# Kernel optimization log

Measured on AMD Instinct MI355X. Metric: run time of the kernel, lower is better.

The kernel has to match this reference:

```python
import jax, jax.numpy as jnp
import numpy as np

B, S, E, H = 4, 2048, 1024, 16
D = E // H  # head dim = 64


def setup_inputs() -> dict:
    key = jax.random.key(0)
    ks = jax.random.split(key, 9)
    s_in = 1.0 / np.sqrt(E)
    return {
        "x": jax.random.normal(ks[0], (B, S, E), dtype=jnp.float32),
        # stacked per-head projection weights, acting as x @ W + b
        "Wq": jax.random.normal(ks[1], (H, E, D), dtype=jnp.float32) * s_in,
        "bq": jax.random.normal(ks[2], (H, D), dtype=jnp.float32) * 0.01,
        "Wk": jax.random.normal(ks[3], (H, E, D), dtype=jnp.float32) * s_in,
        "bk": jax.random.normal(ks[4], (H, D), dtype=jnp.float32) * 0.01,
        "Wv": jax.random.normal(ks[5], (H, E, D), dtype=jnp.float32) * s_in,
        "bv": jax.random.normal(ks[6], (H, D), dtype=jnp.float32) * 0.01,
        "Wo": jax.random.normal(ks[7], (E, E), dtype=jnp.float32) * s_in,
        "bo": jax.random.normal(ks[8], (E,), dtype=jnp.float32) * 0.01,
    }


def reference(x, Wq, bq, Wk, bk, Wv, bv, Wo, bo):
    # Batched per-head projections (equivalent to the per-head nn.Linear loop)
    q = jnp.einsum("bse,hed->bhsd", x, Wq) + bq[None, :, None, :]
    k = jnp.einsum("bse,hed->bhsd", x, Wk) + bk[None, :, None, :]
    v = jnp.einsum("bse,hed->bhsd", x, Wv) + bv[None, :, None, :]
    scale = 1.0 / jnp.sqrt(jnp.asarray(D, dtype=x.dtype))
    scores = jnp.einsum("bhsd,bhtd->bhst", q, k) * scale  # [B,H,S,S]
    attn = jax.nn.softmax(scores, axis=-1)
    ctx = jnp.einsum("bhst,bhtd->bhsd", attn, v)  # [B,H,S,D]
    # torch.cat over heads along last dim -> [B,S,H*D]=[B,S,E]
    ctx = jnp.transpose(ctx, (0, 2, 1, 3)).reshape(x.shape[0], x.shape[1], E)
    return ctx @ Wo + bo
```

## Files before the change

### kernel.cpp

```cpp
#include <hip/hip_runtime.h>
#include <math.h>

#define B_ 4
#define S_ 2048
#define E_ 1024
#define H_ 16
#define D_ 64
#define BH_ (B_ * H_)

#define SCALE_LOG2E 0.18033688011112042f

typedef short short8 __attribute__((ext_vector_type(8)));
typedef float f32x4 __attribute__((ext_vector_type(4)));
typedef float f32x16 __attribute__((ext_vector_type(16)));

static __device__ __forceinline__ unsigned short f2bf(float f) {
    unsigned int u = __float_as_uint(f);
    unsigned int r = (u + 0x7fffu + ((u >> 16) & 1u)) >> 16;
    return (unsigned short)r;
}

static __device__ __forceinline__ unsigned int pack_bf16_trunc(float hi, float lo) {
    return __builtin_amdgcn_perm(__float_as_uint(hi), __float_as_uint(lo), 0x07060302u);
}

static __device__ __forceinline__ void gl_lds16(const unsigned short* g, unsigned short* l) {
    __builtin_amdgcn_global_load_lds(
        (const __attribute__((address_space(1))) unsigned int*)g,
        (__attribute__((address_space(3))) unsigned int*)l, 16, 0, 0);
}


__global__ __launch_bounds__(256) void prep_kernel(
    const float* __restrict__ x, const float* __restrict__ Wq,
    const float* __restrict__ Wk, const float* __restrict__ Wv,
    const float* __restrict__ Wo,
    unsigned short* __restrict__ Xb, unsigned short* __restrict__ Wt,
    unsigned short* __restrict__ Wot)
{
    const int bid = blockIdx.x;
    if (bid < 4096) {
        size_t i = ((size_t)bid * 256 + threadIdx.x) * 8;
        float4 a = *(const float4*)&x[i];
        float4 b = *(const float4*)&x[i + 4];
        ushort4 u0, u1;
        u0.x = f2bf(a.x); u0.y = f2bf(a.y); u0.z = f2bf(a.z); u0.w = f2bf(a.w);
        u1.x = f2bf(b.x); u1.y = f2bf(b.y); u1.z = f2bf(b.z); u1.w = f2bf(b.w);
        *(ushort4*)&Xb[i]     = u0;
        *(ushort4*)&Xb[i + 4] = u1;
        return;
    }
    __shared__ float t[32][33];
    const int tx = threadIdx.x & 31, ty = threadIdx.x >> 5;
    if (bid < 7168) {
        const int idx = bid - 4096;
        const int z = idx >> 6, rem = idx & 63;
        const int r0 = (rem & 31) * 32, c0 = (rem >> 5) * 32;
        const int mtx = z >> 4, h = z & 15;
        const float* s = (mtx == 0 ? Wq : (mtx == 1 ? Wk : Wv)) + (size_t)h * E_ * D_;
        const float scale = (mtx == 0) ? SCALE_LOG2E : 1.0f;
        unsigned short* d = Wt + (size_t)mtx * E_ * E_ + (size_t)h * D_ * E_;
#pragma unroll
        for (int i = 0; i < 4; ++i)
            t[ty + i * 8][tx] = s[(size_t)(r0 + ty + i * 8) * D_ + c0 + tx];
        __syncthreads();
#pragma unroll
        for (int i = 0; i < 4; ++i)
            d[(size_t)(c0 + ty + i * 8) * E_ + r0 + tx] = f2bf(t[tx][ty + i * 8] * scale);
    } else {
        const int idx = bid - 7168;
        const int r0 = (idx & 31) * 32, c0 = (idx >> 5) * 32;
#pragma unroll
        for (int i = 0; i < 4; ++i)
            t[ty + i * 8][tx] = Wo[(size_t)(r0 + ty + i * 8) * E_ + c0 + tx];
        __syncthreads();
#pragma unroll
        for (int i = 0; i < 4; ++i)
            Wot[(size_t)(c0 + ty + i * 8) * E_ + r0 + tx] = f2bf(t[tx][ty + i * 8]);
    }
}

__global__ __launch_bounds__(256, 4) void qkv_gemm_kernel(
    const unsigned short* __restrict__ Xb, const unsigned short* __restrict__ Wt,
    const float* __restrict__ bq, const float* __restrict__ bk,
    const float* __restrict__ bv,
    unsigned short* __restrict__ Qh, unsigned short* __restrict__ Kh,
    unsigned short* __restrict__ Vth)
{
    __shared__ unsigned short As[2][64 * 64];
    __shared__ unsigned short Bs[2][64 * 64];
    const int tid = threadIdx.x;
    const int lane = tid & 63, wid = tid >> 6;
    const int quad = lane >> 4, lc = lane & 15;
    const int wm = wid >> 1, wn = wid & 1;
    const int m0 = blockIdx.y * 128, n0 = blockIdx.x * 128;
    const int l3 = lane >> 3;
    const int cs = (lane & 7) ^ l3;
    const int mloc = 2 * l3 + (cs >> 2);
    const int koff = (cs & 3) * 8;
    const int rdbase = (lc >> 1) * 64 + (((((lc & 1) << 2) | quad) ^ ((lc >> 1) & 7)) << 3);

    f32x4 acc[4][4];
#pragma unroll
    for (int mt = 0; mt < 4; ++mt)
#pragma unroll
        for (int nt = 0; nt < 4; ++nt)
            acc[mt][nt] = (f32x4){0.f, 0.f, 0.f, 0.f};

#pragma unroll
    for (int i = 0; i < 2; ++i) {
        int Rb = wid * 16 + i * 8;
        gl_lds16(&Xb[(size_t)(m0 + Rb * 2 + mloc) * E_ + koff], &As[0][Rb * 64]);
        gl_lds16(&Wt[(size_t)(n0 + Rb * 2 + mloc) * E_ + koff], &Bs[0][Rb * 64]);
    }
    __syncthreads();

    for (int k0 = 0; k0 < E_; k0 += 32) {
        const int cur = (k0 >> 5) & 1;
        if (k0 + 32 < E_) {
#pragma unroll
            for (int i = 0; i < 2; ++i) {
                int Rb = wid * 16 + i * 8;
                gl_lds16(&Xb[(size_t)(m0 + Rb * 2 + mloc) * E_ + k0 + 32 + koff],
                         &As[cur ^ 1][Rb * 64]);
                gl_lds16(&Wt[(size_t)(n0 + Rb * 2 + mloc) * E_ + k0 + 32 + koff],
                         &Bs[cur ^ 1][Rb * 64]);
            }
        }
        short8 a[4], bfr[4];
#pragma unroll
        for (int mt = 0; mt < 4; ++mt)
            a[mt] = *(const short8*)&As[cur][(wm * 32 + mt * 8) * 64 + rdbase];
#pragma unroll
        for (int nt = 0; nt < 4; ++nt)
            bfr[nt] = *(const short8*)&Bs[cur][(wn * 32 + nt * 8) * 64 + rdbase];
#pragma unroll
        for (int mt = 0; mt < 4; ++mt)
#pragma unroll
            for (int nt = 0; nt < 4; ++nt)
                acc[mt][nt] = __builtin_amdgcn_mfma_f32_16x16x32_bf16(
                    a[mt], bfr[nt], acc[mt][nt], 0, 0, 0);
        __syncthreads();
    }

    const int nb = n0 + wn * 64;
    const int mtx = nb >> 10;
    const int h = (nb >> 6) & 15;
    const int sg0 = m0 + wm * 64;
    const int bb_ = sg0 >> 11;
    const int bhv = bb_ * H_ + h;
    if (mtx < 2) {
        const float bsc = (mtx == 0) ? SCALE_LOG2E : 1.0f;
        const float* bias = (mtx == 0 ? bq : bk) + h * D_;
        unsigned short* Out = (mtx == 0) ? Qh : Kh;
        const size_t obase = (size_t)bhv * (S_ / 32) * 2048;
#pragma unroll
        for (int nt = 0; nt < 4; ++nt) {
            int d = nt * 16 + lc;
            int hi_ = (lc >> 3) & 1, j = lc & 7;
            float bb = bias[d] * bsc;
#pragma unroll
            for (int mt = 0; mt < 4; ++mt)
#pragma unroll
                for (int r = 0; r < 4; ++r) {
                    int ss = (sg0 + mt * 16 + quad * 4 + r) & (S_ - 1);
                    Out[obase + ((size_t)(ss >> 5) * 4 + nt) * 512 +
                        ((ss & 31) * 2 + hi_) * 8 + j] = f2bf(acc[mt][nt][r] + bb);
                }
        }
    } else {
        const float* bias = bv + h * D_;
        const size_t obase = (size_t)bhv * (S_ / 64) * 4096;
        const int t64 = (sg0 & (S_ - 1)) >> 6;
        const int hi_ = quad >> 1, j0 = (quad & 1) * 4;
#pragma unroll
        for (int nt = 0; nt < 4; ++nt) {
            int d = nt * 16 + lc;
            int dsub = d >> 5, l31d = d & 31;
            float bb = bias[d];
#pragma unroll
            for (int mt = 0; mt < 4; ++mt) {
                ushort4 u;
                u.x = f2bf(acc[mt][nt][0] + bb);
                u.y = f2bf(acc[mt][nt][1] + bb);
                u.z = f2bf(acc[mt][nt][2] + bb);
                u.w = f2bf(acc[mt][nt][3] + bb);
                *(ushort4*)&Vth[obase + ((size_t)t64 * 8 + mt * 2 + dsub) * 512 +
                                (l31d * 2 + hi_) * 8 + j0] = u;
            }
        }
    }
}

__global__ __launch_bounds__(512, 4) void attn_kernel(
    const unsigned short* __restrict__ Qh, const unsigned short* __restrict__ Kh,
    const unsigned short* __restrict__ Vth, unsigned short* __restrict__ Ch)
{
    __shared__ unsigned short ks[3][8 * 512];
    __shared__ unsigned short vt[3][8 * 512];
    const int tid = threadIdx.x;
    const int lane = tid & 63, wid = tid >> 6;
    const int l31 = lane & 31, hi = lane >> 5;
    const int bh = blockIdx.x, b = bh >> 4, h = bh & 15;
    const int q0 = blockIdx.y * 256;
    const size_t gbase = (size_t)bh * (S_ / 32) * 2048;
    const int rdoff = (l31 * 2 + hi) * 8;
    const int ldoff = lane * 8;

    short8 qf[4];
    {
        const int t32 = (q0 >> 5) + wid;
#pragma unroll
        for (int kc = 0; kc < 4; ++kc)
            qf[kc] = *(const short8*)&Qh[gbase + ((size_t)t32 * 4 + kc) * 512 + rdoff];
    }

#pragma unroll
    for (int tt = 0; tt < 2; ++tt) {
        gl_lds16(&Kh[gbase + ((size_t)(tt * 2 + (wid >> 2)) * 4 + (wid & 3)) * 512 + ldoff],
                 &ks[tt][wid * 512]);
        gl_lds16(&Vth[gbase + ((size_t)tt * 8 + wid) * 512 + ldoff],
                 &vt[tt][wid * 512]);
    }
    __syncthreads();

    f32x16 ctx[2];
    float lsum = 0.f;
#pragma unroll
    for (int i = 0; i < 16; ++i) { ctx[0][i] = 0.f; ctx[1][i] = 0.f; }

    f32x16 stH;
#pragma unroll
    for (int i = 0; i < 16; ++i) stH[i] = 0.f;
#pragma unroll
    for (int kc = 0; kc < 4; ++kc) {
        short8 kf = *(const short8*)&ks[0][kc * 512 + rdoff];
        stH = __builtin_amdgcn_mfma_f32_32x32x16_bf16(kf, qf[kc], stH, 0, 0, 0);
    }

    auto smpv = [&](const f32x16& ST, int buf, int KB) {
#pragma unroll
        for (int ks16 = 0; ks16 < 2; ++ks16) {
            float e0 = __builtin_amdgcn_exp2f(ST[8 * ks16 + 0]);
            float e1 = __builtin_amdgcn_exp2f(ST[8 * ks16 + 1]);
            float e2 = __builtin_amdgcn_exp2f(ST[8 * ks16 + 2]);
            float e3 = __builtin_amdgcn_exp2f(ST[8 * ks16 + 3]);
            float e4 = __builtin_amdgcn_exp2f(ST[8 * ks16 + 4]);
            float e5 = __builtin_amdgcn_exp2f(ST[8 * ks16 + 5]);
            float e6 = __builtin_amdgcn_exp2f(ST[8 * ks16 + 6]);
            float e7 = __builtin_amdgcn_exp2f(ST[8 * ks16 + 7]);
            lsum += ((e0 + e1) + (e2 + e3)) + ((e4 + e5) + (e6 + e7));
            unsigned int w0 = pack_bf16_trunc(e1, e0);
            unsigned int w1 = pack_bf16_trunc(e3, e2);
            unsigned int w2 = pack_bf16_trunc(e5, e4);
            unsigned int w3 = pack_bf16_trunc(e7, e6);
            asm("v_permlane32_swap_b32 %0, %1" : "+v"(w0), "+v"(w2));
            asm("v_permlane32_swap_b32 %0, %1" : "+v"(w1), "+v"(w3));
            union { unsigned int u[4]; short8 s; } pu;
            pu.u[0] = w0; pu.u[1] = w1; pu.u[2] = w2; pu.u[3] = w3;
            const short8 pf = pu.s;
#pragma unroll
            for (int dsub = 0; dsub < 2; ++dsub) {
                short8 vf = *(const short8*)&vt[buf][((KB * 2 + ks16) * 2 + dsub) * 512 + rdoff];
                ctx[dsub] = __builtin_amdgcn_mfma_f32_32x32x16_bf16(
                    pf, vf, ctx[dsub], 0, 0, 0);
            }
        }
    };

    const int NT = S_ / 64;
    for (int t = 0; t < NT; ++t) {
        const int cur = t % 3, nxt = (t + 1) % 3, stg = (t + 2) % 3;
        if (t + 2 < NT) {
            gl_lds16(&Kh[gbase + ((size_t)((t + 2) * 2 + (wid >> 2)) * 4 + (wid & 3)) * 512 + ldoff],
                     &ks[stg][wid * 512]);
            gl_lds16(&Vth[gbase + ((size_t)(t + 2) * 8 + wid) * 512 + ldoff],
                     &vt[stg][wid * 512]);
        }

        f32x16 stN;
#pragma unroll
        for (int i = 0; i < 16; ++i) stN[i] = 0.f;
        __builtin_amdgcn_s_setprio(1);
#pragma unroll
        for (int kc = 0; kc < 4; ++kc) {
            short8 kf = *(const short8*)&ks[cur][(4 + kc) * 512 + rdoff];
            stN = __builtin_amdgcn_mfma_f32_32x32x16_bf16(kf, qf[kc], stN, 0, 0, 0);
        }
        __builtin_amdgcn_s_setprio(0);
        smpv(stH, cur, 0);
        stH = stN;

#pragma unroll
        for (int i = 0; i < 16; ++i) stN[i] = 0.f;
        if (t + 1 < NT) {
            __builtin_amdgcn_s_setprio(1);
#pragma unroll
            for (int kc = 0; kc < 4; ++kc) {
                short8 kf = *(const short8*)&ks[nxt][kc * 512 + rdoff];
                stN = __builtin_amdgcn_mfma_f32_32x32x16_bf16(kf, qf[kc], stN, 0, 0, 0);
            }
            __builtin_amdgcn_s_setprio(0);
        }
        smpv(stH, cur, 1);
        stH = stN;

        __syncthreads();
    }

    float* lsh = (float*)&ks[0][0];
    {
        float a = lsum, bx = lsum;
        asm("v_permlane32_swap_b32 %0, %1" : "+v"(a), "+v"(bx));
        float ltot = lsum + (hi ? a : bx);
        if (hi == 0) lsh[wid * 32 + l31] = ltot;
    }
    __syncthreads();
#pragma unroll
    for (int r = 0; r < 16; ++r) {
        int qr = (r & 3) + ((r >> 2) << 3) + hi * 4;
        float inv = 1.f / lsh[wid * 32 + qr];
        int q = q0 + wid * 32 + qr;
        size_t rowbase = ((size_t)b * S_ + q) * E_ + h * D_;
        Ch[rowbase + l31]      = f2bf(ctx[0][r] * inv);
        Ch[rowbase + 32 + l31] = f2bf(ctx[1][r] * inv);
    }
}

__global__ __launch_bounds__(256, 4) void out_proj_kernel(
    const unsigned short* __restrict__ Ch, const unsigned short* __restrict__ Wot,
    const float* __restrict__ bo, float* __restrict__ out)
{
    __shared__ unsigned short As[2][64 * 64];
    __shared__ unsigned short Bs[2][64 * 64];
    const int tid = threadIdx.x;
    const int lane = tid & 63, wid = tid >> 6;
    const int quad = lane >> 4, lc = lane & 15;
    const int wm = wid >> 1, wn = wid & 1;
    const int m0 = blockIdx.y * 128, n0 = blockIdx.x * 128;
    const int l3 = lane >> 3;
    const int cs = (lane & 7) ^ l3;
    const int mloc = 2 * l3 + (cs >> 2);
    const int koff = (cs & 3) * 8;
    const int rdbase = (lc >> 1) * 64 + (((((lc & 1) << 2) | quad) ^ ((lc >> 1) & 7)) << 3);

    f32x4 acc[4][4];
#pragma unroll
    for (int mt = 0; mt < 4; ++mt)
#pragma unroll
        for (int nt = 0; nt < 4; ++nt)
            acc[mt][nt] = (f32x4){0.f, 0.f, 0.f, 0.f};

#pragma unroll
    for (int i = 0; i < 2; ++i) {
        int Rb = wid * 16 + i * 8;
        gl_lds16(&Ch[(size_t)(m0 + Rb * 2 + mloc) * E_ + koff], &As[0][Rb * 64]);
        gl_lds16(&Wot[(size_t)(n0 + Rb * 2 + mloc) * E_ + koff], &Bs[0][Rb * 64]);
    }
    __syncthreads();

    for (int k0 = 0; k0 < E_; k0 += 32) {
        const int cur = (k0 >> 5) & 1;
        if (k0 + 32 < E_) {
#pragma unroll
            for (int i = 0; i < 2; ++i) {
                int Rb = wid * 16 + i * 8;
                gl_lds16(&Ch[(size_t)(m0 + Rb * 2 + mloc) * E_ + k0 + 32 + koff],
                         &As[cur ^ 1][Rb * 64]);
                gl_lds16(&Wot[(size_t)(n0 + Rb * 2 + mloc) * E_ + k0 + 32 + koff],
                         &Bs[cur ^ 1][Rb * 64]);
            }
        }
        short8 a[4], bfr[4];
#pragma unroll
        for (int mt = 0; mt < 4; ++mt)
            a[mt] = *(const short8*)&As[cur][(wm * 32 + mt * 8) * 64 + rdbase];
#pragma unroll
        for (int nt = 0; nt < 4; ++nt)
            bfr[nt] = *(const short8*)&Bs[cur][(wn * 32 + nt * 8) * 64 + rdbase];
#pragma unroll
        for (int mt = 0; mt < 4; ++mt)
#pragma unroll
            for (int nt = 0; nt < 4; ++nt)
                acc[mt][nt] = __builtin_amdgcn_mfma_f32_16x16x32_bf16(
                    a[mt], bfr[nt], acc[mt][nt], 0, 0, 0);
        __syncthreads();
    }

#pragma unroll
    for (int mt = 0; mt < 4; ++mt)
#pragma unroll
        for (int nt = 0; nt < 4; ++nt) {
            int n = n0 + wn * 64 + nt * 16 + lc;
            float bb = bo[n];
#pragma unroll
            for (int r = 0; r < 4; ++r) {
                int row = m0 + wm * 64 + mt * 16 + quad * 4 + r;
                out[(size_t)row * E_ + n] = acc[mt][nt][r] + bb;
            }
        }
}

extern "C" void kernel_launch(void* const* d_in, const int* in_sizes, int n_in,
                              void* d_out, int out_size, void* d_ws, size_t ws_size,
                              hipStream_t stream)
{
    const float* x  = (const float*)d_in[0];
    const float* Wq = (const float*)d_in[1];
    const float* bq = (const float*)d_in[2];
    const float* Wk = (const float*)d_in[3];
    const float* bk = (const float*)d_in[4];
    const float* Wv = (const float*)d_in[5];
    const float* bv = (const float*)d_in[6];
    const float* Wo = (const float*)d_in[7];
    const float* bo = (const float*)d_in[8];
    (void)in_sizes; (void)n_in; (void)out_size; (void)ws_size;

    const size_t N = (size_t)BH_ * S_ * D_;
    unsigned short* Wt  = (unsigned short*)d_ws;
    unsigned short* Wot = Wt + (size_t)3072 * 1024;
    unsigned short* Xb  = Wot + (size_t)1024 * 1024;
    unsigned short* Qh  = Xb + N;
    unsigned short* Kh  = Qh + N;
    unsigned short* Vth = Kh + N;
    unsigned short* Ch  = Vth + N;

    prep_kernel<<<dim3(8192), 256, 0, stream>>>(x, Wq, Wk, Wv, Wo, Xb, Wt, Wot);
    qkv_gemm_kernel<<<dim3(24, 64), 256, 0, stream>>>(Xb, Wt, bq, bk, bv, Qh, Kh, Vth);
    attn_kernel<<<dim3(64, 8), 512, 0, stream>>>(Qh, Kh, Vth, Ch);
    out_proj_kernel<<<dim3(8, 64), 256, 0, stream>>>(Ch, Wot, bo, (float*)d_out);
}
```

Measured before the change: 268.4 us.

## Triple-buffer LDS staging in QKV and output projection GEMMs with explicit vmcnt waits

Both projection GEMMs move from a double-buffered to a three-stage LDS ring, prefetching two k-tiles ahead. `__syncthreads` is replaced by explicit `s_waitcnt vmcnt` counts plus raw `s_barrier` and sched_barrier fences, so only the oldest tile's loads must land before compute. The aim is to hide more global-load latency behind the MFMAs. In exchange LDS per block grows and the launch-bounds occupancy hint drops from 4 to 3, and correctness depends on the hard-coded vmcnt counts matching the number of load instructions `gl_lds16` actually emits.

```diff
diff --git a/kernel.cpp b/kernel.cpp
--- a/kernel.cpp
+++ b/kernel.cpp
@@ -80,15 +80,15 @@
     }
 }
 
-__global__ __launch_bounds__(256, 4) void qkv_gemm_kernel(
+__global__ __launch_bounds__(256, 3) void qkv_gemm_kernel(
     const unsigned short* __restrict__ Xb, const unsigned short* __restrict__ Wt,
     const float* __restrict__ bq, const float* __restrict__ bk,
     const float* __restrict__ bv,
     unsigned short* __restrict__ Qh, unsigned short* __restrict__ Kh,
     unsigned short* __restrict__ Vth)
 {
-    __shared__ unsigned short As[2][64 * 64];
-    __shared__ unsigned short Bs[2][64 * 64];
+    __shared__ unsigned short As[3][64 * 64];
+    __shared__ unsigned short Bs[3][64 * 64];
     const int tid = threadIdx.x;
     const int lane = tid & 63, wid = tid >> 6;
     const int quad = lane >> 4, lc = lane & 15;
@@ -108,25 +108,34 @@
             acc[mt][nt] = (f32x4){0.f, 0.f, 0.f, 0.f};
 
 #pragma unroll
-    for (int i = 0; i < 2; ++i) {
-        int Rb = wid * 16 + i * 8;
-        gl_lds16(&Xb[(size_t)(m0 + Rb * 2 + mloc) * E_ + koff], &As[0][Rb * 64]);
-        gl_lds16(&Wt[(size_t)(n0 + Rb * 2 + mloc) * E_ + koff], &Bs[0][Rb * 64]);
-    }
-    __syncthreads();
-
-    for (int k0 = 0; k0 < E_; k0 += 32) {
-        const int cur = (k0 >> 5) & 1;
-        if (k0 + 32 < E_) {
+    for (int tt = 0; tt < 2; ++tt)
+#pragma unroll
+        for (int i = 0; i < 2; ++i) {
+            int Rb = wid * 16 + i * 8;
+            gl_lds16(&Xb[(size_t)(m0 + Rb * 2 + mloc) * E_ + tt * 32 + koff], &As[tt][Rb * 64]);
+            gl_lds16(&Wt[(size_t)(n0 + Rb * 2 + mloc) * E_ + tt * 32 + koff], &Bs[tt][Rb * 64]);
+        }
+
+    const int NT = E_ / 32;
+    for (int t = 0; t < NT; ++t) {
+        const int cur = t % 3, stg = (t + 2) % 3;
+        if (t + 2 < NT) {
+            const int ko = (t + 2) * 32;
 #pragma unroll
             for (int i = 0; i < 2; ++i) {
                 int Rb = wid * 16 + i * 8;
-                gl_lds16(&Xb[(size_t)(m0 + Rb * 2 + mloc) * E_ + k0 + 32 + koff],
-                         &As[cur ^ 1][Rb * 64]);
-                gl_lds16(&Wt[(size_t)(n0 + Rb * 2 + mloc) * E_ + k0 + 32 + koff],
-                         &Bs[cur ^ 1][Rb * 64]);
-            }
-        }
+                gl_lds16(&Xb[(size_t)(m0 + Rb * 2 + mloc) * E_ + ko + koff], &As[stg][Rb * 64]);
+                gl_lds16(&Wt[(size_t)(n0 + Rb * 2 + mloc) * E_ + ko + koff], &Bs[stg][Rb * 64]);
+            }
+            asm volatile("s_waitcnt vmcnt(8)" ::: "memory");
+        } else if (t + 1 < NT) {
+            asm volatile("s_waitcnt vmcnt(4)" ::: "memory");
+        } else {
+            asm volatile("s_waitcnt vmcnt(0)" ::: "memory");
+        }
+        __builtin_amdgcn_s_barrier();
+        __builtin_amdgcn_sched_barrier(0);
+
         short8 a[4], bfr[4];
 #pragma unroll
         for (int mt = 0; mt < 4; ++mt)
@@ -140,7 +149,9 @@
             for (int nt = 0; nt < 4; ++nt)
                 acc[mt][nt] = __builtin_amdgcn_mfma_f32_16x16x32_bf16(
                     a[mt], bfr[nt], acc[mt][nt], 0, 0, 0);
-        __syncthreads();
+
+        __builtin_amdgcn_sched_barrier(0);
+        __builtin_amdgcn_s_barrier();
     }
 
     const int nb = n0 + wn * 64;
@@ -327,12 +338,12 @@
     }
 }
 
-__global__ __launch_bounds__(256, 4) void out_proj_kernel(
+__global__ __launch_bounds__(256, 3) void out_proj_kernel(
     const unsigned short* __restrict__ Ch, const unsigned short* __restrict__ Wot,
     const float* __restrict__ bo, float* __restrict__ out)
 {
-    __shared__ unsigned short As[2][64 * 64];
-    __shared__ unsigned short Bs[2][64 * 64];
+    __shared__ unsigned short As[3][64 * 64];
+    __shared__ unsigned short Bs[3][64 * 64];
     const int tid = threadIdx.x;
     const int lane = tid & 63, wid = tid >> 6;
     const int quad = lane >> 4, lc = lane & 15;
@@ -352,25 +363,34 @@
             acc[mt][nt] = (f32x4){0.f, 0.f, 0.f, 0.f};
 
 #pragma unroll
-    for (int i = 0; i < 2; ++i) {
-        int Rb = wid * 16 + i * 8;
-        gl_lds16(&Ch[(size_t)(m0 + Rb * 2 + mloc) * E_ + koff], &As[0][Rb * 64]);
-        gl_lds16(&Wot[(size_t)(n0 + Rb * 2 + mloc) * E_ + koff], &Bs[0][Rb * 64]);
-    }
-    __syncthreads();
-
-    for (int k0 = 0; k0 < E_; k0 += 32) {
-        const int cur = (k0 >> 5) & 1;
-        if (k0 + 32 < E_) {
+    for (int tt = 0; tt < 2; ++tt)
+#pragma unroll
+        for (int i = 0; i < 2; ++i) {
+            int Rb = wid * 16 + i * 8;
+            gl_lds16(&Ch[(size_t)(m0 + Rb * 2 + mloc) * E_ + tt * 32 + koff], &As[tt][Rb * 64]);
+            gl_lds16(&Wot[(size_t)(n0 + Rb * 2 + mloc) * E_ + tt * 32 + koff], &Bs[tt][Rb * 64]);
+        }
+
+    const int NT = E_ / 32;
+    for (int t = 0; t < NT; ++t) {
+        const int cur = t % 3, stg = (t + 2) % 3;
+        if (t + 2 < NT) {
+            const int ko = (t + 2) * 32;
 #pragma unroll
             for (int i = 0; i < 2; ++i) {
                 int Rb = wid * 16 + i * 8;
-                gl_lds16(&Ch[(size_t)(m0 + Rb * 2 + mloc) * E_ + k0 + 32 + koff],
-                         &As[cur ^ 1][Rb * 64]);
-                gl_lds16(&Wot[(size_t)(n0 + Rb * 2 + mloc) * E_ + k0 + 32 + koff],
-                         &Bs[cur ^ 1][Rb * 64]);
-            }
-        }
+                gl_lds16(&Ch[(size_t)(m0 + Rb * 2 + mloc) * E_ + ko + koff], &As[stg][Rb * 64]);
+                gl_lds16(&Wot[(size_t)(n0 + Rb * 2 + mloc) * E_ + ko + koff], &Bs[stg][Rb * 64]);
+            }
+            asm volatile("s_waitcnt vmcnt(8)" ::: "memory");
+        } else if (t + 1 < NT) {
+            asm volatile("s_waitcnt vmcnt(4)" ::: "memory");
+        } else {
+            asm volatile("s_waitcnt vmcnt(0)" ::: "memory");
+        }
+        __builtin_amdgcn_s_barrier();
+        __builtin_amdgcn_sched_barrier(0);
+
         short8 a[4], bfr[4];
 #pragma unroll
         for (int mt = 0; mt < 4; ++mt)
@@ -384,7 +404,9 @@
             for (int nt = 0; nt < 4; ++nt)
                 acc[mt][nt] = __builtin_amdgcn_mfma_f32_16x16x32_bf16(
                     a[mt], bfr[nt], acc[mt][nt], 0, 0, 0);
-        __syncthreads();
+
+        __builtin_amdgcn_sched_barrier(0);
+        __builtin_amdgcn_s_barrier();
     }
 
 #pragma unroll
```

New measurement: 264.6 us. Within noise of the previous version (-1.4%).
